# Kernel tuning notes

Measured on AMD Instinct MI355X. Metric: run time of the kernel, lower is better.

## Reference

```python
import jax, jax.numpy as jnp
import numpy as np
from math import gcd


def _get_start_index(length):
    if length <= 2:
        return 0
    return (length - 1) // 2


def setup_inputs() -> dict:
    key = jax.random.key(0)
    k1, k2 = jax.random.split(key)
    N = 8388608          # signal length (2^23 samples)
    F = 1023             # FIR taps
    x = jax.random.normal(k1, (N,), dtype=jnp.float32)
    filter_coeffs = jax.random.normal(k2, (F,), dtype=jnp.float32)
    return {"x": x, "up": 3, "down": 2, "filter_coeffs": filter_coeffs}


def reference(x, up, down, filter_coeffs):
    # Reduce the rational ratio (static Python ints)
    g = gcd(up, down)
    up = up // g
    down = down // g

    N = x.shape[0]
    F = filter_coeffs.shape[0]

    # Zero-stuff: x_up[::up] = up * x  -> length up*N
    x_up = jnp.zeros(up * N, dtype=x.dtype).at[::up].set(up * x)

    start = _get_start_index(F)
    out_len = (N * up) // down + bool((N * up) % down)

    if up == 1 and down == 1:
        return x_up[:out_len]

    # torch.conv1d(x_up, flip(h), padding=F-1) == full convolution np.convolve(x_up, h)
    full = jnp.convolve(x_up, filter_coeffs, mode="full")  # length up*N + F - 1
    x_out = full[start::down]
    return x_out[:out_len]
```

## Files before the change

### kernel.cpp

```cpp
#include <hip/hip_runtime.h>


typedef __attribute__((ext_vector_type(8))) short bf16x8;
typedef __attribute__((ext_vector_type(4))) float f32x4;

constexpr int SBLK = 4096;
constexpr int TPW  = 4;
constexpr int NQ   = 12;
constexpr int XW   = 8576;
constexpr int XSEG = XW / 8;
constexpr int HHN  = 416;
constexpr int OBW  = 3168;

constexpr int SMEM_BYTES = 4 * OBW * 4;

__device__ __forceinline__ unsigned short f2bf(float f) {
    union { float f; unsigned int u; } c; c.f = f;
    unsigned int u = c.u;
    return (unsigned short)((u + 0x7FFFu + ((u >> 16) & 1u)) >> 16);
}
__device__ __forceinline__ int swz(int seg) { return seg ^ ((seg >> 3) & 7); }
__device__ __forceinline__ int swp(int i)   { return i + (i >> 5); }

__global__ __launch_bounds__(256)
void resample_mfma_kernel(const float* __restrict__ x,
                          const float* __restrict__ h,
                          float* __restrict__ out, int N)
{
    __shared__ __align__(16) char smem[SMEM_BYTES];
    unsigned short* xr = (unsigned short*)smem;
    unsigned short* hh = (unsigned short*)(smem + 17152);
    float* obuf = (float*)smem;

    const int tid = threadIdx.x;
    const int s0  = blockIdx.x * SBLK;
    const int GHI = 2 * s0 + 8363;

    for (int i = tid; i < 3 * HHN; i += 256) {
        const int r   = i / HHN;
        const int t   = (i - r * HHN) - 32;
        const int hix = (r == 0) ? 3 * t - 2 : ((r == 1) ? 3 * t : 3 * t + 2);
        const float v = (t >= 0 && hix >= 0 && hix < 1023) ? 3.0f * h[hix] : 0.0f;
        hh[i] = f2bf(v);
    }

    for (int st = tid; st < XSEG; st += 256) {
        const int g7 = GHI - 8 * st - 7;
        float f[8];
        if (g7 >= 0 && g7 + 7 < N) {
            const float4 lo = *reinterpret_cast<const float4*>(x + g7);
            const float4 hi = *reinterpret_cast<const float4*>(x + g7 + 4);
            f[0] = hi.w; f[1] = hi.z; f[2] = hi.y; f[3] = hi.x;
            f[4] = lo.w; f[5] = lo.z; f[6] = lo.y; f[7] = lo.x;
        } else {
            #pragma unroll
            for (int e = 0; e < 8; ++e) {
                const int idx = GHI - 8 * st - e;
                f[e] = (idx >= 0 && idx < N) ? x[idx] : 0.0f;
            }
        }
        uint4 w;
        w.x = (unsigned)f2bf(f[0]) | ((unsigned)f2bf(f[1]) << 16);
        w.y = (unsigned)f2bf(f[2]) | ((unsigned)f2bf(f[3]) << 16);
        w.z = (unsigned)f2bf(f[4]) | ((unsigned)f2bf(f[5]) << 16);
        w.w = (unsigned)f2bf(f[6]) | ((unsigned)f2bf(f[7]) << 16);
        *reinterpret_cast<uint4*>(xr + 8 * swz(st)) = w;
    }
    __syncthreads();

    const int wave = tid >> 6;
    const int lane = tid & 63;
    const int n    = lane & 15;
    const int quad = lane >> 4;

    f32x4 acc[TPW][3] = {};

    const unsigned int* hw = (const unsigned int*)hh;

    #pragma unroll 3
    for (int q = 0; q < NQ; ++q) {
        bf16x8 A[3];
        #pragma unroll
        for (int r = 0; r < 3; ++r) {
            const int w0 = r * 208 + 16 * q + n + 4 * quad;
            uint4 aw;
            aw.x = hw[w0]; aw.y = hw[w0 + 1]; aw.z = hw[w0 + 2]; aw.w = hw[w0 + 3];
            A[r] = __builtin_bit_cast(bf16x8, aw);
        }
        #pragma unroll
        for (int jj = 0; jj < TPW; ++jj) {
            const int tile = wave * TPW + jj;
            const int seg  = 1020 - 64 * tile - 4 * n + 4 * q + quad;
            const uint4 bw = *reinterpret_cast<const uint4*>(xr + 8 * swz(seg));
            const bf16x8 B = __builtin_bit_cast(bf16x8, bw);
            #pragma unroll
            for (int r = 0; r < 3; ++r)
                acc[jj][r] = __builtin_amdgcn_mfma_f32_16x16x32_bf16(A[r], B, acc[jj][r], 0, 0, 0);
        }
    }

    __syncthreads();

    float* ob = obuf + wave * OBW;
    #pragma unroll
    for (int jj = 0; jj < TPW; ++jj)
        #pragma unroll
        for (int r = 0; r < 3; ++r)
            #pragma unroll
            for (int i = 0; i < 4; ++i) {
                const int off = 3 * (256 * jj + 4 * quad + i + 16 * n) + r;
                ob[swp(off)] = acc[jj][r][i];
            }
    __syncthreads();

    const int obase = 3 * s0 + 3072 * wave;
    #pragma unroll
    for (int it = 0; it < 12; ++it) {
        const int t4 = (it * 64 + lane) * 4;
        float4 v;
        v.x = ob[swp(t4)];
        v.y = ob[swp(t4 + 1)];
        v.z = ob[swp(t4 + 2)];
        v.w = ob[swp(t4 + 3)];
        *reinterpret_cast<float4*>(out + obase + t4) = v;
    }
}

extern "C" void kernel_launch(void* const* d_in, const int* in_sizes, int n_in,
                              void* d_out, int out_size, void* d_ws, size_t ws_size,
                              hipStream_t stream)
{
    const float* x = (const float*)d_in[0];
    const float* h = (const float*)d_in[3];
    float* out = (float*)d_out;

    const int N    = in_sizes[0];
    const int S    = out_size / 3;
    const int nblk = S / SBLK;

    resample_mfma_kernel<<<nblk, 256, 0, stream>>>(x, h, out, N);
}
```

Baseline: 104.0 us.

## Prepack filter MFMA fragments in LDS and vectorize output staging

Filter coefficients are now laid out in shared memory directly in per-lane MFMA A-fragment order, so each A operand becomes a single 16-byte LDS read instead of four scalar reads. The main loop is fully unrolled. The epilogue writes accumulators to LDS as float4 chunks per lane and reads them back with an index remap for coalesced global stores, replacing the scalar padded scatter and gather. This adds a larger shared-memory footprint (about 54KB vs 51KB) and more index arithmetic in the epilogue and in the fragment-building prologue.

```diff
diff --git a/kernel.cpp b/kernel.cpp
--- a/kernel.cpp
+++ b/kernel.cpp
@@ -7,12 +7,10 @@
 constexpr int SBLK = 4096;
 constexpr int TPW  = 4;
 constexpr int NQ   = 12;
-constexpr int XW   = 8576;
-constexpr int XSEG = XW / 8;
-constexpr int HHN  = 416;
-constexpr int OBW  = 3168;
+constexpr int XSEG = 1072;
+constexpr int AFN  = 3 * NQ * 64;
 
-constexpr int SMEM_BYTES = 4 * OBW * 4;
+constexpr int SMEM_BYTES = 17152 + 36864;
 
 __device__ __forceinline__ unsigned short f2bf(float f) {
     union { float f; unsigned int u; } c; c.f = f;
@@ -20,7 +18,6 @@
     return (unsigned short)((u + 0x7FFFu + ((u >> 16) & 1u)) >> 16);
 }
 __device__ __forceinline__ int swz(int seg) { return seg ^ ((seg >> 3) & 7); }
-__device__ __forceinline__ int swp(int i)   { return i + (i >> 5); }
 
 __global__ __launch_bounds__(256)
 void resample_mfma_kernel(const float* __restrict__ x,
@@ -29,19 +26,33 @@
 {
     __shared__ __align__(16) char smem[SMEM_BYTES];
     unsigned short* xr = (unsigned short*)smem;
-    unsigned short* hh = (unsigned short*)(smem + 17152);
-    float* obuf = (float*)smem;
+    uint4* afr  = (uint4*)(smem + 17152);
+    float4* ob4 = (float4*)smem;
 
     const int tid = threadIdx.x;
     const int s0  = blockIdx.x * SBLK;
     const int GHI = 2 * s0 + 8363;
 
-    for (int i = tid; i < 3 * HHN; i += 256) {
-        const int r   = i / HHN;
-        const int t   = (i - r * HHN) - 32;
-        const int hix = (r == 0) ? 3 * t - 2 : ((r == 1) ? 3 * t : 3 * t + 2);
-        const float v = (t >= 0 && hix >= 0 && hix < 1023) ? 3.0f * h[hix] : 0.0f;
-        hh[i] = f2bf(v);
+    for (int e = tid; e < AFN; e += 256) {
+        const int r   = e / 768;
+        const int rem = e - r * 768;
+        const int q   = rem >> 6;
+        const int le  = rem & 63;
+        const int Tb  = 32 * q + 2 * (le & 15) + 8 * (le >> 4);
+        unsigned int w[4];
+        #pragma unroll
+        for (int jp = 0; jp < 4; ++jp) {
+            unsigned short half[2];
+            #pragma unroll
+            for (int u = 0; u < 2; ++u) {
+                const int t   = Tb + 2 * jp + u - 32;
+                const int hix = (r == 0) ? 3 * t - 2 : ((r == 1) ? 3 * t : 3 * t + 2);
+                half[u] = (t >= 0 && hix >= 0 && hix < 1023) ? f2bf(3.0f * h[hix])
+                                                             : (unsigned short)0;
+            }
+            w[jp] = (unsigned)half[0] | ((unsigned)half[1] << 16);
+        }
+        afr[e] = make_uint4(w[0], w[1], w[2], w[3]);
     }
 
     for (int st = tid; st < XSEG; st += 256) {
@@ -75,24 +86,18 @@
 
     f32x4 acc[TPW][3] = {};
 
-    const unsigned int* hw = (const unsigned int*)hh;
-
-    #pragma unroll 3
+    #pragma unroll
     for (int q = 0; q < NQ; ++q) {
         bf16x8 A[3];
         #pragma unroll
-        for (int r = 0; r < 3; ++r) {
-            const int w0 = r * 208 + 16 * q + n + 4 * quad;
-            uint4 aw;
-            aw.x = hw[w0]; aw.y = hw[w0 + 1]; aw.z = hw[w0 + 2]; aw.w = hw[w0 + 3];
-            A[r] = __builtin_bit_cast(bf16x8, aw);
-        }
+        for (int r = 0; r < 3; ++r)
+            A[r] = __builtin_bit_cast(bf16x8, afr[(r * 12 + q) * 64 + lane]);
         #pragma unroll
         for (int jj = 0; jj < TPW; ++jj) {
             const int tile = wave * TPW + jj;
             const int seg  = 1020 - 64 * tile - 4 * n + 4 * q + quad;
-            const uint4 bw = *reinterpret_cast<const uint4*>(xr + 8 * swz(seg));
-            const bf16x8 B = __builtin_bit_cast(bf16x8, bw);
+            const bf16x8 B = __builtin_bit_cast(
+                bf16x8, *reinterpret_cast<const uint4*>(xr + 8 * swz(seg)));
             #pragma unroll
             for (int r = 0; r < 3; ++r)
                 acc[jj][r] = __builtin_amdgcn_mfma_f32_16x16x32_bf16(A[r], B, acc[jj][r], 0, 0, 0);
@@ -101,28 +106,34 @@
 
     __syncthreads();
 
-    float* ob = obuf + wave * OBW;
     #pragma unroll
-    for (int jj = 0; jj < TPW; ++jj)
+    for (int jj = 0; jj < TPW; ++jj) {
+        const int T  = wave * TPW + jj;
+        const int cb = (T * 64 + lane) * 3;
+        float v[12];
         #pragma unroll
         for (int r = 0; r < 3; ++r)
             #pragma unroll
-            for (int i = 0; i < 4; ++i) {
-                const int off = 3 * (256 * jj + 4 * quad + i + 16 * n) + r;
-                ob[swp(off)] = acc[jj][r][i];
-            }
+            for (int i = 0; i < 4; ++i)
+                v[3 * i + r] = acc[jj][r][i];
+        #pragma unroll
+        for (int j = 0; j < 3; ++j)
+            ob4[cb + j] = make_float4(v[4 * j], v[4 * j + 1], v[4 * j + 2], v[4 * j + 3]);
+    }
     __syncthreads();
 
-    const int obase = 3 * s0 + 3072 * wave;
+    const int obase = 3 * s0;
     #pragma unroll
     for (int it = 0; it < 12; ++it) {
-        const int t4 = (it * 64 + lane) * 4;
-        float4 v;
-        v.x = ob[swp(t4)];
-        v.y = ob[swp(t4 + 1)];
-        v.z = ob[swp(t4 + 2)];
-        v.w = ob[swp(t4 + 3)];
-        *reinterpret_cast<float4*>(out + obase + t4) = v;
+        const int o   = it * 1024 + 4 * tid;
+        const int T   = o / 768;
+        const int w2  = o - 768 * T;
+        const int nn  = w2 / 48;
+        const int rm  = w2 - 48 * nn;
+        const int qd  = rm / 12;
+        const int dd  = rm - 12 * qd;
+        const float4 val = ob4[(T * 64 + 16 * qd + nn) * 3 + (dd >> 2)];
+        *reinterpret_cast<float4*>(out + obase + o) = val;
     }
 }
 
```

Result: slower. 118.5 us (+14.0%).
